# Kernel tuning notes

Hardware: AMD Instinct MI355X
Metric: run time of the kernel (lower is better)

Reference implementation:

```python
import jax, jax.numpy as jnp
import numpy as np

BN_EPS = 1e-5

def setup_inputs() -> dict:
    key = jax.random.key(0)
    ks = jax.random.split(key, 16)
    B, N = 64, 1024
    dims = [3, 64, 128, 256]
    H = 256
    inp = {"x": jax.random.normal(ks[0], (B, dims[0], N), dtype=jnp.float32)}
    for i in range(3):
        ci, co = dims[i], dims[i + 1]
        inp[f"w{i+1}"] = jax.random.normal(ks[1 + i], (co, ci), dtype=jnp.float32) * (1.0 / np.sqrt(ci))
        inp[f"b{i+1}"] = jnp.zeros((co,), dtype=jnp.float32)
        inp[f"g{i+1}"] = jnp.ones((co,), dtype=jnp.float32)
        inp[f"be{i+1}"] = jnp.zeros((co,), dtype=jnp.float32)
    inp["A"] = jnp.eye(H, dtype=jnp.float32) + 0.01 * jax.random.normal(ks[10], (H, H), dtype=jnp.float32)
    inp["Bm"] = 0.01 * jax.random.normal(ks[11], (H, dims[-1]), dtype=jnp.float32)
    inp["Cm"] = 0.01 * jax.random.normal(ks[12], (dims[-1], H), dtype=jnp.float32)
    return inp


def _conv_bn_relu(h, w, b, g, be):
    # h: [B, Cin, N]; 1x1 conv == channel matmul
    y = jnp.einsum('oi,bin->bon', w, h) + b[None, :, None]
    mu = jnp.mean(y, axis=(0, 2), keepdims=True)
    var = jnp.var(y, axis=(0, 2), keepdims=True)
    y = (y - mu) * jax.lax.rsqrt(var + BN_EPS)
    y = y * g[None, :, None] + be[None, :, None]
    return jax.nn.relu(y)


def reference(x, w1, b1, g1, be1, w2, b2, g2, be2, w3, b3, g3, be3, A, Bm, Cm):
    h = _conv_bn_relu(x, w1, b1, g1, be1)
    h = _conv_bn_relu(h, w2, b2, g2, be2)
    h = _conv_bn_relu(h, w3, b3, g3, be3)
    u = jnp.transpose(h, (0, 2, 1))  # [B, N, C]
    Bsz = u.shape[0]
    H = A.shape[0]
    A_norm = A / (jnp.linalg.norm(A, ord=2) + 1e-5)
    uB = u @ Bm.T  # precompute input projection: [B, N, H]

    def step(hstate, ut):
        hstate = jax.nn.relu(hstate @ A_norm.T + ut)
        return hstate, hstate @ Cm.T

    h0 = jnp.zeros((Bsz, H), dtype=x.dtype)
    _, ys = jax.lax.scan(step, h0, jnp.transpose(uB, (1, 0, 2)))  # ys: [N, B, Cout]
    y = jnp.transpose(ys, (1, 2, 0))  # [B, Cout, N]
    return y
```

## Files before the change

kernel.cpp:

```cpp
#include <hip/hip_runtime.h>

#define B_SZ 64
#define N_SZ 1024
#define C1   64
#define C2   128
#define C3   256
#define H_SZ 256

__global__ void k_btb(const float* __restrict__ A, float* __restrict__ B0) {
  int i = blockIdx.x;
  int j = threadIdx.x;
  float acc = 0.f;
  for (int k = 0; k < 256; ++k)
    acc = fmaf(A[k * 256 + i], A[k * 256 + j], acc);
  B0[i * 256 + j] = acc;
}

__global__ void k_bsq(const float* __restrict__ Bin, float* __restrict__ Bout) {
  __shared__ float diag[256];
  int i = blockIdx.x, j = threadIdx.x;
  diag[j] = Bin[j * 256 + j];
  __syncthreads();
  float tr = 0.f;
  for (int k = 0; k < 256; ++k) tr += diag[k];
  float inv = 1.0f / tr;
  float acc = 0.f;
  for (int k = 0; k < 256; ++k)
    acc = fmaf(Bin[i * 256 + k], Bin[k * 256 + j], acc);
  Bout[i * 256 + j] = acc * inv * inv;
}

__global__ void k_sfin(const float* __restrict__ Bf, const float* __restrict__ B0,
                       float* __restrict__ sinv) {
  __shared__ float v[256], w[256];
  __shared__ float red[256];
  __shared__ int redi[256];
  int t = threadIdx.x;
  red[t] = Bf[t * 256 + t];
  redi[t] = t;
  __syncthreads();
  for (int s = 128; s > 0; s >>= 1) {
    if (t < s) {
      if (red[t + s] > red[t]) { red[t] = red[t + s]; redi[t] = redi[t + s]; }
    }
    __syncthreads();
  }
  int jmax = redi[0];
  __syncthreads();
  v[t] = Bf[t * 256 + jmax];
  __syncthreads();
  float acc = 0.f;
  for (int k = 0; k < 256; ++k) acc = fmaf(B0[t * 256 + k], v[k], acc);
  w[t] = acc;
  __syncthreads();
  red[t] = v[t] * w[t];
  __syncthreads();
  for (int s = 128; s > 0; s >>= 1) { if (t < s) red[t] += red[t + s]; __syncthreads(); }
  float num = red[0];
  __syncthreads();
  red[t] = v[t] * v[t];
  __syncthreads();
  for (int s = 128; s > 0; s >>= 1) { if (t < s) red[t] += red[t + s]; __syncthreads(); }
  if (t == 0) {
    float lam = num / red[0];
    float sg = sqrtf(lam);
    *sinv = 1.0f / (sg + 1e-5f);
  }
}

__global__ void k_conv1(const float* __restrict__ x, const float* __restrict__ w,
                        const float* __restrict__ bias, float* __restrict__ y) {
  int b = blockIdx.x >> 2;
  int n = ((blockIdx.x & 3) << 8) + threadIdx.x;
  const float* xb = x + (size_t)b * 3 * N_SZ;
  float x0 = xb[n], x1 = xb[N_SZ + n], x2 = xb[2 * N_SZ + n];
  float* yb = y + (size_t)b * C1 * N_SZ;
#pragma unroll 4
  for (int o = 0; o < C1; ++o) {
    float r = fmaf(w[o * 3 + 0], x0,
              fmaf(w[o * 3 + 1], x1,
              fmaf(w[o * 3 + 2], x2, bias[o])));
    yb[(size_t)o * N_SZ + n] = r;
  }
}

__global__ void k_stats(const float* __restrict__ y, int C,
                        const float* __restrict__ g, const float* __restrict__ be,
                        float* __restrict__ coef) {
  int c = blockIdx.x;
  int t = threadIdx.x;
  float s1 = 0.f, s2 = 0.f;
  for (int b = 0; b < B_SZ; ++b) {
    const float4* p = (const float4*)(y + ((size_t)b * C + c) * N_SZ);
    float4 v = p[t];
    s1 += v.x + v.y + v.z + v.w;
    s2 += v.x * v.x + v.y * v.y + v.z * v.z + v.w * v.w;
  }
  __shared__ float r1[256], r2[256];
  r1[t] = s1; r2[t] = s2;
  __syncthreads();
  for (int s = 128; s > 0; s >>= 1) {
    if (t < s) { r1[t] += r1[t + s]; r2[t] += r2[t + s]; }
    __syncthreads();
  }
  if (t == 0) {
    const float M = (float)(B_SZ * N_SZ);
    float mu = r1[0] / M;
    float var = r2[0] / M - mu * mu;
    float sc = g[c] * rsqrtf(var + 1e-5f);
    coef[c] = sc;
    coef[C + c] = be[c] - mu * sc;
  }
}

template <int K, int CO>
__global__ void k_conv(const float* __restrict__ hin, const float* __restrict__ coef,
                       const float* __restrict__ w, const float* __restrict__ bias,
                       float* __restrict__ y) {
  __shared__ float wt2[16][68];
  __shared__ float ht[16][68];
  int b = blockIdx.x, ot = blockIdx.y, nt = blockIdx.z;
  int t = threadIdx.x;
  int tx = t & 15, ty = t >> 4;
  float acc[4][4] = {};
  const float* hb = hin + (size_t)b * K * N_SZ + nt * 64;
  for (int k0 = 0; k0 < K; k0 += 16) {
    {
      int r = t >> 2, cc = (t & 3) * 4;
      float4 v = *(const float4*)(w + (size_t)(ot * 64 + r) * K + k0 + cc);
      wt2[cc + 0][r] = v.x; wt2[cc + 1][r] = v.y;
      wt2[cc + 2][r] = v.z; wt2[cc + 3][r] = v.w;
    }
    {
      int r = t >> 4, cc = (t & 15) * 4;
      float sc = coef[k0 + r], sh = coef[K + k0 + r];
      const float* hp = hb + (size_t)(k0 + r) * N_SZ + cc;
      float4 v;
      v.x = fmaxf(fmaf(hp[0], sc, sh), 0.f);
      v.y = fmaxf(fmaf(hp[1], sc, sh), 0.f);
      v.z = fmaxf(fmaf(hp[2], sc, sh), 0.f);
      v.w = fmaxf(fmaf(hp[3], sc, sh), 0.f);
      *(float4*)&ht[r][cc] = v;
    }
    __syncthreads();
#pragma unroll
    for (int k = 0; k < 16; ++k) {
      float4 hv = *(const float4*)&ht[k][tx * 4];
      float4 wv = *(const float4*)&wt2[k][ty * 4];
      float hvv[4] = {hv.x, hv.y, hv.z, hv.w};
      float wvv[4] = {wv.x, wv.y, wv.z, wv.w};
#pragma unroll
      for (int i = 0; i < 4; ++i)
#pragma unroll
        for (int j = 0; j < 4; ++j) acc[i][j] = fmaf(wvv[i], hvv[j], acc[i][j]);
    }
    __syncthreads();
  }
  float* yb = y + ((size_t)b * CO + ot * 64) * N_SZ + nt * 64;
#pragma unroll
  for (int i = 0; i < 4; ++i) {
    float bv = bias[ot * 64 + ty * 4 + i];
    float4 v;
    v.x = acc[i][0] + bv; v.y = acc[i][1] + bv;
    v.z = acc[i][2] + bv; v.w = acc[i][3] + bv;
    *(float4*)(yb + (size_t)(ty * 4 + i) * N_SZ + tx * 4) = v;
  }
}

__global__ void k_uB(const float* __restrict__ y3, const float* __restrict__ coef,
                     const float* __restrict__ Bm, float* __restrict__ uB) {
  __shared__ float xt[32][68];
  __shared__ float bt2[32][68];
  int b = blockIdx.x, nt = blockIdx.y, htile = blockIdx.z;
  int t = threadIdx.x, tx = t & 15, ty = t >> 4;
  float acc[4][4] = {};
  const float* yb = y3 + (size_t)b * C3 * N_SZ + nt * 64;
  for (int c0 = 0; c0 < C3; c0 += 32) {
#pragma unroll
    for (int rr = 0; rr < 2; ++rr) {
      int r = (t >> 4) + rr * 16;
      int cidx = c0 + r;
      float sc = coef[cidx], sh = coef[C3 + cidx];
      int cc = (t & 15) * 4;
      const float* p = yb + (size_t)cidx * N_SZ + cc;
      float4 v;
      v.x = fmaxf(fmaf(p[0], sc, sh), 0.f);
      v.y = fmaxf(fmaf(p[1], sc, sh), 0.f);
      v.z = fmaxf(fmaf(p[2], sc, sh), 0.f);
      v.w = fmaxf(fmaf(p[3], sc, sh), 0.f);
      *(float4*)&xt[r][cc] = v;
    }
#pragma unroll
    for (int rr = 0; rr < 2; ++rr) {
      int r = (t >> 3) + rr * 32;
      int cc = (t & 7) * 4;
      float4 v = *(const float4*)(Bm + (size_t)(htile * 64 + r) * H_SZ + c0 + cc);
      bt2[cc + 0][r] = v.x; bt2[cc + 1][r] = v.y;
      bt2[cc + 2][r] = v.z; bt2[cc + 3][r] = v.w;
    }
    __syncthreads();
#pragma unroll
    for (int k = 0; k < 32; ++k) {
      float4 xv = *(const float4*)&xt[k][ty * 4];
      float4 bv = *(const float4*)&bt2[k][tx * 4];
      float xvv[4] = {xv.x, xv.y, xv.z, xv.w};
      float bvv[4] = {bv.x, bv.y, bv.z, bv.w};
#pragma unroll
      for (int i = 0; i < 4; ++i)
#pragma unroll
        for (int j = 0; j < 4; ++j) acc[i][j] = fmaf(bvv[i], xvv[j], acc[i][j]);
    }
    __syncthreads();
  }
  float* ob = uB + (size_t)b * N_SZ * H_SZ;
#pragma unroll
  for (int j = 0; j < 4; ++j) {
    float4 v;
    v.x = acc[0][j]; v.y = acc[1][j]; v.z = acc[2][j]; v.w = acc[3][j];
    *(float4*)(ob + (size_t)(nt * 64 + ty * 4 + j) * H_SZ + htile * 64 + tx * 4) = v;
  }
}

__global__ __launch_bounds__(512, 1) void k_scan(
    const float* __restrict__ A, const float* __restrict__ sinvp,
    const float* __restrict__ uB, float* __restrict__ hs) {
  __shared__ float h_lds[256];
  __shared__ float part[8][256];
  const int b = blockIdx.x;
  const int t = threadIdx.x;
  const int lane = t & 63;
  const int wv = t >> 6;
  const float sinv = *sinvp;
  float areg[4][32];
#pragma unroll
  for (int k = 0; k < 4; ++k) {
    const float* r = A + (size_t)(lane + 64 * k) * 256 + wv * 32;
#pragma unroll
    for (int j = 0; j < 32; ++j) areg[k][j] = r[j] * sinv;
  }
  if (t < 256) h_lds[t] = 0.f;
  __syncthreads();
  const float* ub = uB + (size_t)b * N_SZ * H_SZ;
  float* ho = hs + (size_t)b * N_SZ * H_SZ;
  float u_cur = (t < 256) ? ub[t] : 0.f;
  for (int s = 0; s < N_SZ; ++s) {
    float u_next = 0.f;
    if (t < 256 && s + 1 < N_SZ) u_next = ub[(size_t)(s + 1) * H_SZ + t];
    const float4* hp = ((const float4*)h_lds) + wv * 8;
    float acc[4] = {0.f, 0.f, 0.f, 0.f};
#pragma unroll
    for (int q = 0; q < 8; ++q) {
      const float4 h4 = hp[q];
#pragma unroll
      for (int k = 0; k < 4; ++k) {
        acc[k] = fmaf(areg[k][q * 4 + 0], h4.x, acc[k]);
        acc[k] = fmaf(areg[k][q * 4 + 1], h4.y, acc[k]);
        acc[k] = fmaf(areg[k][q * 4 + 2], h4.z, acc[k]);
        acc[k] = fmaf(areg[k][q * 4 + 3], h4.w, acc[k]);
      }
    }
    part[wv][lane] = acc[0];
    part[wv][lane + 64] = acc[1];
    part[wv][lane + 128] = acc[2];
    part[wv][lane + 192] = acc[3];
    asm volatile("s_waitcnt lgkmcnt(0)" ::: "memory");
    __builtin_amdgcn_s_barrier();
    if (t < 256) {
      float p = u_cur;
#pragma unroll
      for (int c = 0; c < 8; ++c) p += part[c][t];
      p = fmaxf(p, 0.f);
      h_lds[t] = p;
      ho[(size_t)s * H_SZ + t] = p;
    }
    u_cur = u_next;
    asm volatile("s_waitcnt lgkmcnt(0)" ::: "memory");
    __builtin_amdgcn_s_barrier();
  }
}

__global__ void k_ymm(const float* __restrict__ hs, const float* __restrict__ Cm,
                      float* __restrict__ y) {
  __shared__ float st2[32][68];
  __shared__ float ct2[32][68];
  int b = blockIdx.x, ot = blockIdx.y, nt = blockIdx.z;
  int t = threadIdx.x, tx = t & 15, ty = t >> 4;
  float acc[4][4] = {};
  const float* hb = hs + (size_t)b * N_SZ * H_SZ + (size_t)nt * 64 * H_SZ;
  for (int h0 = 0; h0 < H_SZ; h0 += 32) {
#pragma unroll
    for (int rr = 0; rr < 2; ++rr) {
      int r = (t >> 3) + rr * 32;
      int cc = (t & 7) * 4;
      float4 v = *(const float4*)(hb + (size_t)r * H_SZ + h0 + cc);
      st2[cc + 0][r] = v.x; st2[cc + 1][r] = v.y;
      st2[cc + 2][r] = v.z; st2[cc + 3][r] = v.w;
    }
#pragma unroll
    for (int rr = 0; rr < 2; ++rr) {
      int r = (t >> 3) + rr * 32;
      int cc = (t & 7) * 4;
      float4 v = *(const float4*)(Cm + (size_t)(ot * 64 + r) * H_SZ + h0 + cc);
      ct2[cc + 0][r] = v.x; ct2[cc + 1][r] = v.y;
      ct2[cc + 2][r] = v.z; ct2[cc + 3][r] = v.w;
    }
    __syncthreads();
#pragma unroll
    for (int k = 0; k < 32; ++k) {
      float4 sv = *(const float4*)&st2[k][tx * 4];
      float4 cv = *(const float4*)&ct2[k][ty * 4];
      float svv[4] = {sv.x, sv.y, sv.z, sv.w};
      float cvv[4] = {cv.x, cv.y, cv.z, cv.w};
#pragma unroll
      for (int i = 0; i < 4; ++i)
#pragma unroll
        for (int j = 0; j < 4; ++j) acc[i][j] = fmaf(cvv[i], svv[j], acc[i][j]);
    }
    __syncthreads();
  }
  float* yb = y + ((size_t)b * C3 + ot * 64) * N_SZ + nt * 64;
#pragma unroll
  for (int i = 0; i < 4; ++i) {
    float4 v;
    v.x = acc[i][0]; v.y = acc[i][1]; v.z = acc[i][2]; v.w = acc[i][3];
    *(float4*)(yb + (size_t)(ty * 4 + i) * N_SZ + tx * 4) = v;
  }
}

extern "C" void kernel_launch(void* const* d_in, const int* in_sizes, int n_in,
                              void* d_out, int out_size, void* d_ws, size_t ws_size,
                              hipStream_t stream) {
  const float* x   = (const float*)d_in[0];
  const float* w1  = (const float*)d_in[1];
  const float* b1  = (const float*)d_in[2];
  const float* g1  = (const float*)d_in[3];
  const float* be1 = (const float*)d_in[4];
  const float* w2  = (const float*)d_in[5];
  const float* b2  = (const float*)d_in[6];
  const float* g2  = (const float*)d_in[7];
  const float* be2 = (const float*)d_in[8];
  const float* w3  = (const float*)d_in[9];
  const float* b3  = (const float*)d_in[10];
  const float* g3  = (const float*)d_in[11];
  const float* be3 = (const float*)d_in[12];
  const float* A   = (const float*)d_in[13];
  const float* Bm  = (const float*)d_in[14];
  const float* Cm  = (const float*)d_in[15];
  float* out = (float*)d_out;

  char* ws = (char*)d_ws;
  const size_t MB = 1024ull * 1024ull;
  float* y1 = (float*)(ws + 0);
  float* y2 = (float*)(ws + 16 * MB);
  float* y3 = (float*)(ws + 48 * MB);
  float* hs = (float*)(ws + 0);
  char* sp = ws + 112 * MB;
  float* B0 = (float*)(sp);
  float* P  = (float*)(sp + 256 * 1024);
  float* Q  = (float*)(sp + 512 * 1024);
  float* sinv  = (float*)(sp + 768 * 1024);
  float* coef1 = (float*)(sp + 768 * 1024 + 1024);
  float* coef2 = (float*)(sp + 768 * 1024 + 4096);
  float* coef3 = (float*)(sp + 768 * 1024 + 8192);

  k_btb<<<256, 256, 0, stream>>>(A, B0);
  {
    float* bufs[2] = {P, Q};
    const float* cur = B0;
    for (int it = 0; it < 12; ++it) {
      float* nxt = bufs[it & 1];
      k_bsq<<<256, 256, 0, stream>>>(cur, nxt);
      cur = nxt;
    }
    k_sfin<<<1, 256, 0, stream>>>(cur, B0, sinv);
  }

  k_conv1<<<dim3(B_SZ * 4), 256, 0, stream>>>(x, w1, b1, y1);
  k_stats<<<C1, 256, 0, stream>>>(y1, C1, g1, be1, coef1);
  k_conv<C1, C2><<<dim3(B_SZ, C2 / 64, N_SZ / 64), 256, 0, stream>>>(y1, coef1, w2, b2, y2);
  k_stats<<<C2, 256, 0, stream>>>(y2, C2, g2, be2, coef2);
  k_conv<C2, C3><<<dim3(B_SZ, C3 / 64, N_SZ / 64), 256, 0, stream>>>(y2, coef2, w3, b3, y3);
  k_stats<<<C3, 256, 0, stream>>>(y3, C3, g3, be3, coef3);

  k_uB<<<dim3(B_SZ, N_SZ / 64, H_SZ / 64), 256, 0, stream>>>(y3, coef3, Bm, out);

  k_scan<<<dim3(B_SZ), 512, 0, stream>>>(A, sinv, out, hs);

  k_ymm<<<dim3(B_SZ, C3 / 64, N_SZ / 64), 256, 0, stream>>>(hs, Cm, out);
}
```

Before: 1.097 ms.

## Restructure scan step to keep hidden state in registers with one barrier per step

```diff
diff --git a/kernel.cpp b/kernel.cpp
--- a/kernel.cpp
+++ b/kernel.cpp
@@ -221,61 +221,65 @@
   }
 }
 
-__global__ __launch_bounds__(512, 1) void k_scan(
+__device__ __forceinline__ float dpp_xor1(float x) {
+  int i = __builtin_amdgcn_update_dpp(0, __float_as_int(x), 0xB1, 0xF, 0xF, true);
+  return __int_as_float(i);
+}
+
+__global__ __launch_bounds__(512, 2) void k_scan(
     const float* __restrict__ A, const float* __restrict__ sinvp,
     const float* __restrict__ uB, float* __restrict__ hs) {
-  __shared__ float h_lds[256];
-  __shared__ float part[8][256];
+  __shared__ float part2[2][256][12];
   const int b = blockIdx.x;
   const int t = threadIdx.x;
   const int lane = t & 63;
   const int wv = t >> 6;
   const float sinv = *sinvp;
-  float areg[4][32];
-#pragma unroll
-  for (int k = 0; k < 4; ++k) {
-    const float* r = A + (size_t)(lane + 64 * k) * 256 + wv * 32;
-#pragma unroll
-    for (int j = 0; j < 32; ++j) areg[k][j] = r[j] * sinv;
-  }
-  if (t < 256) h_lds[t] = 0.f;
-  __syncthreads();
+  float a0[32], a1[32], a2[32], a3[32];
+  {
+    const float* r0 = A + (size_t)(lane) * 256 + wv * 32;
+    const float* r1 = A + (size_t)(lane + 64) * 256 + wv * 32;
+    const float* r2 = A + (size_t)(lane + 128) * 256 + wv * 32;
+    const float* r3 = A + (size_t)(lane + 192) * 256 + wv * 32;
+#pragma unroll
+    for (int j = 0; j < 32; ++j) {
+      a0[j] = r0[j] * sinv; a1[j] = r1[j] * sinv;
+      a2[j] = r2[j] * sinv; a3[j] = r3[j] * sinv;
+    }
+  }
+  const int i_r = wv * 32 + (lane >> 1);
   const float* ub = uB + (size_t)b * N_SZ * H_SZ;
   float* ho = hs + (size_t)b * N_SZ * H_SZ;
-  float u_cur = (t < 256) ? ub[t] : 0.f;
+  float v_h = 0.f;
+  float u_cur = ub[i_r];
   for (int s = 0; s < N_SZ; ++s) {
     float u_next = 0.f;
-    if (t < 256 && s + 1 < N_SZ) u_next = ub[(size_t)(s + 1) * H_SZ + t];
-    const float4* hp = ((const float4*)h_lds) + wv * 8;
-    float acc[4] = {0.f, 0.f, 0.f, 0.f};
-#pragma unroll
-    for (int q = 0; q < 8; ++q) {
-      const float4 h4 = hp[q];
-#pragma unroll
-      for (int k = 0; k < 4; ++k) {
-        acc[k] = fmaf(areg[k][q * 4 + 0], h4.x, acc[k]);
-        acc[k] = fmaf(areg[k][q * 4 + 1], h4.y, acc[k]);
-        acc[k] = fmaf(areg[k][q * 4 + 2], h4.z, acc[k]);
-        acc[k] = fmaf(areg[k][q * 4 + 3], h4.w, acc[k]);
-      }
-    }
-    part[wv][lane] = acc[0];
-    part[wv][lane + 64] = acc[1];
-    part[wv][lane + 128] = acc[2];
-    part[wv][lane + 192] = acc[3];
+    if (s + 1 < N_SZ) u_next = ub[(size_t)(s + 1) * H_SZ + i_r];
+    float acc0 = 0.f, acc1 = 0.f, acc2 = 0.f, acc3 = 0.f;
+#pragma unroll
+    for (int p = 0; p < 32; ++p) {
+      const float hv =
+          __int_as_float(__builtin_amdgcn_readlane(__float_as_int(v_h), 2 * p));
+      acc0 = fmaf(a0[p], hv, acc0);
+      acc1 = fmaf(a1[p], hv, acc1);
+      acc2 = fmaf(a2[p], hv, acc2);
+      acc3 = fmaf(a3[p], hv, acc3);
+    }
+    const int buf = s & 1;
+    part2[buf][lane][wv] = acc0;
+    part2[buf][lane + 64][wv] = acc1;
+    part2[buf][lane + 128][wv] = acc2;
+    part2[buf][lane + 192][wv] = acc3;
     asm volatile("s_waitcnt lgkmcnt(0)" ::: "memory");
     __builtin_amdgcn_s_barrier();
-    if (t < 256) {
-      float p = u_cur;
-#pragma unroll
-      for (int c = 0; c < 8; ++c) p += part[c][t];
-      p = fmaxf(p, 0.f);
-      h_lds[t] = p;
-      ho[(size_t)s * H_SZ + t] = p;
-    }
+    __builtin_amdgcn_sched_barrier(0);
+    const float4 pr = *(const float4*)&part2[buf][i_r][(lane & 1) * 4];
+    float sum = (pr.x + pr.y) + (pr.z + pr.w);
+    sum += dpp_xor1(sum);
+    float pv = fmaxf(sum + u_cur, 0.f);
+    v_h = pv;
+    if ((lane & 1) == 0) ho[(size_t)s * H_SZ + i_r] = pv;
     u_cur = u_next;
-    asm volatile("s_waitcnt lgkmcnt(0)" ::: "memory");
-    __builtin_amdgcn_s_barrier();
   }
 }
 
```

Measured after the change: 1.454 ms. 1.33x slower.
